# Optimization experiments

Hardware: AMD Instinct MI355X
Metric: run time of the kernel (lower is better)

## Reference

```python
import jax, jax.numpy as jnp
import numpy as np

B, T, D, E, K = 8, 4096, 1024, 64, 2


def setup_inputs() -> dict:
    key = jax.random.key(0)
    k1, k2, k3, k4 = jax.random.split(key, 4)
    return {
        "mh_output": jax.random.normal(k1, (B, T, D), dtype=jnp.float32),
        "W_route": jax.random.normal(k2, (D, E), dtype=jnp.float32) * (1.0 / np.sqrt(D)),
        "b_route": jnp.zeros((E,), dtype=jnp.float32),
        "W_noise": jax.random.normal(k3, (D, E), dtype=jnp.float32) * (1.0 / np.sqrt(D)),
        "b_noise": jnp.zeros((E,), dtype=jnp.float32),
        "noise_u": jax.random.uniform(k4, (B, T, E), dtype=jnp.float32),
        "top_k": K,
    }


def reference(mh_output, W_route, b_route, W_noise, b_noise, noise_u, top_k):
    # [B,T,D] @ [D,E] -> [B,T,E]
    logits = jnp.einsum("btd,de->bte", mh_output, W_route) + b_route
    noise_logits = jnp.einsum("btd,de->bte", mh_output, W_noise) + b_noise
    noisy_logits = logits + noise_u * jax.nn.softplus(noise_logits)
    # top-k over experts
    top_k_logits, indices = jax.lax.top_k(noisy_logits, top_k)  # [B,T,K]
    # scatter top-k values back into -inf canvas == mask non-topk to -inf
    mask = jax.nn.one_hot(indices, E, dtype=jnp.bool_).any(axis=-2)  # [B,T,E]
    sparse_logits = jnp.where(mask, noisy_logits, -jnp.inf)
    router_output = jax.nn.softmax(sparse_logits, axis=-1)
    return (router_output, indices)
```

## Files before the change

kernel.cpp:

```cpp
#include <hip/hip_runtime.h>
#include <math.h>

#define MROWS 32768
#define DDIM  1024
#define EDIM  64
#define NCH   64
#define TILEM 32

typedef _Float16 f16x8 __attribute__((ext_vector_type(8)));
typedef float    f32x16 __attribute__((ext_vector_type(16)));

__global__ __launch_bounds__(256)
void convW_kernel(const float* __restrict__ Wr, const float* __restrict__ Wn,
                  unsigned short* __restrict__ ws) {
    int gid = blockIdx.x * 256 + threadIdx.x;
    int c32 = gid & 31;
    int j   = (gid >> 5) & 7;
    int lhi = (gid >> 8) & 1;
    int nf  = (gid >> 9) & 3;
    int c   = gid >> 11;
    int lane = lhi * 32 + c32;
    int k   = c * 16 + lhi * 8 + j;
    int col = nf * 32 + c32;
    float w = (col < EDIM) ? Wr[k * EDIM + col] : Wn[k * EDIM + (col - EDIM)];
    _Float16 hi = (_Float16)w;
    _Float16 lo = (_Float16)((w - (float)hi) * 2048.0f);
    union { _Float16 h; unsigned short u; } cv;
    size_t base = (size_t)c * 4096 + nf * 512 + lane * 8 + j;
    cv.h = hi; ws[base]        = cv.u;
    cv.h = lo; ws[base + 2048] = cv.u;
}

__global__ __launch_bounds__(256, 4)
void router_mfma(const float* __restrict__ X,
                 const unsigned short* __restrict__ WS,
                 const float* __restrict__ br_g,
                 const float* __restrict__ bn_g,
                 const float* __restrict__ U,
                 float* __restrict__ out)
{
    __shared__ alignas(16) unsigned char smem[22528];
    unsigned short* Ah = (unsigned short*)smem;
    unsigned short* Bh = (unsigned short*)(smem + 6144);
    float*          Lf = (float*)smem;

    const int t    = threadIdx.x;
    const int lane = t & 63;
    const int wid  = t >> 6;
    const int rowBase = blockIdx.x * TILEM;
    const int start   = (blockIdx.x & 7) * 8;

    const int arow = t >> 3;
    const int akk  = (t & 7) * 2;
    const float* xbase = X + (size_t)(rowBase + arow) * DDIM + akk;

    f32x16 acc0, acc1;
#pragma unroll
    for (int i = 0; i < 16; ++i) { acc0[i] = 0.f; acc1[i] = 0.f; }

    auto stageB = [&](int c, int buf) {
        const char* src = (const char*)WS + (size_t)c * 8192 + wid * 2048 + lane * 16;
        char* dst = (char*)(smem + 6144) + buf * 8192 + wid * 2048 + lane * 16;
        __builtin_amdgcn_global_load_lds(
            (const __attribute__((address_space(1))) void*)src,
            (__attribute__((address_space(3))) void*)dst, 16, 0, 0);
        __builtin_amdgcn_global_load_lds(
            (const __attribute__((address_space(1))) void*)(src + 1024),
            (__attribute__((address_space(3))) void*)(dst + 1024), 16, 0, 0);
    };

    auto convA = [&](float2 xv, int buf) {
        _Float16 h0 = (_Float16)xv.x;
        _Float16 h1 = (_Float16)xv.y;
        _Float16 l0 = (_Float16)((xv.x - (float)h0) * 2048.0f);
        _Float16 l1 = (_Float16)((xv.y - (float)h1) * 2048.0f);
        union { _Float16 h[2]; unsigned int u; } ph, pl;
        ph.h[0] = h0; ph.h[1] = h1; pl.h[0] = l0; pl.h[1] = l1;
        *(unsigned int*)(Ah + ((buf * 2 + 0) * 32 + arow) * 24 + akk) = ph.u;
        *(unsigned int*)(Ah + ((buf * 2 + 1) * 32 + arow) * 24 + akk) = pl.u;
    };

    auto compute = [&](int buf) {
        const unsigned short* Ab = Ah + (buf * 2) * 768;
        const int aoff = (lane & 31) * 24 + (lane >> 5) * 8;
        f16x8 ahi = *(const f16x8*)(Ab + aoff);
        f16x8 alo = *(const f16x8*)(Ab + 768 + aoff);
        const unsigned short* Bb = Bh + buf * 4096 + wid * 512 + lane * 8;
        f16x8 bhi = *(const f16x8*)(Bb);
        f16x8 blo = *(const f16x8*)(Bb + 2048);
        acc0 = __builtin_amdgcn_mfma_f32_32x32x16_f16(ahi, bhi, acc0, 0, 0, 0);
        acc1 = __builtin_amdgcn_mfma_f32_32x32x16_f16(ahi, blo, acc1, 0, 0, 0);
        acc1 = __builtin_amdgcn_mfma_f32_32x32x16_f16(alo, bhi, acc1, 0, 0, 0);
    };

    float2 xA = *(const float2*)(xbase + (size_t)start * 16);
    stageB(start, 0);
    convA(xA, 0);
    xA = *(const float2*)(xbase + (size_t)((start + 1) & 63) * 16);
    float2 xB = *(const float2*)(xbase + (size_t)((start + 2) & 63) * 16);
    __syncthreads();

#define PHASE(I, CUR, NXT)                                                     \
    {                                                                          \
        const int buf = (I) & 1;                                               \
        if ((I) + 1 < NCH) stageB((start + (I) + 1) & 63, buf ^ 1);            \
        float2 tmp = CUR;                                                      \
        if ((I) + 3 < NCH)                                                     \
            tmp = *(const float2*)(xbase + (size_t)((start + (I) + 3) & 63) * 16); \
        compute(buf);                                                          \
        if ((I) + 1 < NCH) convA(CUR, buf ^ 1);                                \
        CUR = tmp;                                                             \
        __syncthreads();                                                       \
    }

    for (int i = 0; i < NCH; i += 2) {
        PHASE(i,     xA, xB);
        PHASE(i + 1, xB, xA);
    }
#undef PHASE

    const float inv2048 = 1.0f / 2048.0f;
    const int lcol = wid * 32 + (lane & 31);
#pragma unroll
    for (int reg = 0; reg < 16; ++reg) {
        int r = (reg & 3) + 8 * (reg >> 2) + 4 * (lane >> 5);
        Lf[r * 132 + lcol] = acc0[reg] + acc1[reg] * inv2048;
    }
    __syncthreads();

    const float brv = br_g[lane];
    const float bnv = bn_g[lane];
#pragma unroll 2
    for (int r8 = 0; r8 < 8; ++r8) {
        int lrow = wid * 8 + r8;
        int grow = rowBase + lrow;
        float lr = Lf[lrow * 132 + lane] + brv;
        float ln = Lf[lrow * 132 + 64 + lane] + bnv;
        float u  = U[(size_t)grow * EDIM + lane];
        float noisy = lr + u * log1pf(expf(ln));

        float m1 = noisy; int i1 = lane;
        float m2 = -INFINITY; int i2 = 64;
#pragma unroll
        for (int s = 1; s < 64; s <<= 1) {
            float om1 = __shfl_xor(m1, s); int oi1 = __shfl_xor(i1, s);
            float om2 = __shfl_xor(m2, s); int oi2 = __shfl_xor(i2, s);
            bool aw = (m1 > om1) || (m1 == om1 && i1 < oi1);
            float w1  = aw ? m1 : om1;  int wi1  = aw ? i1 : oi1;
            float c2a = aw ? m2 : om2;  int c2ai = aw ? i2 : oi2;
            float c2b = aw ? om1 : m1;  int c2bi = aw ? oi1 : i1;
            bool bw = (c2b > c2a) || (c2b == c2a && c2bi < c2ai);
            m1 = w1; i1 = wi1;
            m2 = bw ? c2b : c2a;
            i2 = bw ? c2bi : c2ai;
        }
        float e2  = expf(m2 - m1);
        float inv = 1.0f / (1.0f + e2);
        float p   = (lane == i1) ? inv : ((lane == i2) ? e2 * inv : 0.0f);
        out[(size_t)grow * EDIM + lane] = p;
        if (lane < 2)
            out[(size_t)MROWS * EDIM + (size_t)grow * 2 + lane] =
                (float)(lane == 0 ? i1 : i2);
    }
}

extern "C" void kernel_launch(void* const* d_in, const int* in_sizes, int n_in,
                              void* d_out, int out_size, void* d_ws, size_t ws_size,
                              hipStream_t stream) {
    const float* X  = (const float*)d_in[0];
    const float* Wr = (const float*)d_in[1];
    const float* br = (const float*)d_in[2];
    const float* Wn = (const float*)d_in[3];
    const float* bn = (const float*)d_in[4];
    const float* U  = (const float*)d_in[5];
    (void)in_sizes; (void)n_in; (void)ws_size;
    unsigned short* ws16 = (unsigned short*)d_ws;
    convW_kernel<<<512, 256, 0, stream>>>(Wr, Wn, ws16);
    router_mfma<<<MROWS / TILEM, 256, 0, stream>>>(X, ws16, br, bn, U, (float*)d_out);
}
```

Baseline: 62.41 us.

## Deepen B-tile prefetch to a 4-slot LDS ring with manual waitcnt barriers

Grows the B staging area into a four-slot ring so each weight chunk is issued two iterations ahead instead of one. The X loads become a two-deep register prefetch. The generic __syncthreads is replaced with an explicit partial vmcnt wait plus s_barrier, so later loads can stay in flight across the barrier. MFMA issue is wrapped in s_setprio to favour matrix instructions. This hides more global latency but raises LDS use from about 22KB to about 38KB per block, which may limit occupancy. It also depends on exact vmcnt accounting, which has no margin for error.

```diff
diff --git a/kernel.cpp b/kernel.cpp
--- a/kernel.cpp
+++ b/kernel.cpp
@@ -39,7 +39,7 @@
                  const float* __restrict__ U,
                  float* __restrict__ out)
 {
-    __shared__ alignas(16) unsigned char smem[22528];
+    __shared__ alignas(16) unsigned char smem[38912];
     unsigned short* Ah = (unsigned short*)smem;
     unsigned short* Bh = (unsigned short*)(smem + 6144);
     float*          Lf = (float*)smem;
@@ -58,9 +58,9 @@
 #pragma unroll
     for (int i = 0; i < 16; ++i) { acc0[i] = 0.f; acc1[i] = 0.f; }
 
-    auto stageB = [&](int c, int buf) {
+    auto stageB = [&](int c, int ring) {
         const char* src = (const char*)WS + (size_t)c * 8192 + wid * 2048 + lane * 16;
-        char* dst = (char*)(smem + 6144) + buf * 8192 + wid * 2048 + lane * 16;
+        char* dst = (char*)(smem + 6144) + ring * 8192 + wid * 2048 + lane * 16;
         __builtin_amdgcn_global_load_lds(
             (const __attribute__((address_space(1))) void*)src,
             (__attribute__((address_space(3))) void*)dst, 16, 0, 0);
@@ -69,55 +69,63 @@
             (__attribute__((address_space(3))) void*)(dst + 1024), 16, 0, 0);
     };
 
-    auto convA = [&](float2 xv, int buf) {
+    auto convA = [&](float2 xv, int abuf) {
         _Float16 h0 = (_Float16)xv.x;
         _Float16 h1 = (_Float16)xv.y;
         _Float16 l0 = (_Float16)((xv.x - (float)h0) * 2048.0f);
         _Float16 l1 = (_Float16)((xv.y - (float)h1) * 2048.0f);
         union { _Float16 h[2]; unsigned int u; } ph, pl;
         ph.h[0] = h0; ph.h[1] = h1; pl.h[0] = l0; pl.h[1] = l1;
-        *(unsigned int*)(Ah + ((buf * 2 + 0) * 32 + arow) * 24 + akk) = ph.u;
-        *(unsigned int*)(Ah + ((buf * 2 + 1) * 32 + arow) * 24 + akk) = pl.u;
+        *(unsigned int*)(Ah + ((abuf * 2 + 0) * 32 + arow) * 24 + akk) = ph.u;
+        *(unsigned int*)(Ah + ((abuf * 2 + 1) * 32 + arow) * 24 + akk) = pl.u;
     };
 
-    auto compute = [&](int buf) {
-        const unsigned short* Ab = Ah + (buf * 2) * 768;
+    auto compute = [&](int abuf, int ring) {
+        const unsigned short* Ab = Ah + abuf * 1536;
         const int aoff = (lane & 31) * 24 + (lane >> 5) * 8;
         f16x8 ahi = *(const f16x8*)(Ab + aoff);
         f16x8 alo = *(const f16x8*)(Ab + 768 + aoff);
-        const unsigned short* Bb = Bh + buf * 4096 + wid * 512 + lane * 8;
+        const unsigned short* Bb = Bh + ring * 4096 + wid * 512 + lane * 8;
         f16x8 bhi = *(const f16x8*)(Bb);
         f16x8 blo = *(const f16x8*)(Bb + 2048);
+        __builtin_amdgcn_s_setprio(1);
         acc0 = __builtin_amdgcn_mfma_f32_32x32x16_f16(ahi, bhi, acc0, 0, 0, 0);
         acc1 = __builtin_amdgcn_mfma_f32_32x32x16_f16(ahi, blo, acc1, 0, 0, 0);
         acc1 = __builtin_amdgcn_mfma_f32_32x32x16_f16(alo, bhi, acc1, 0, 0, 0);
+        __builtin_amdgcn_s_setprio(0);
     };
 
-    float2 xA = *(const float2*)(xbase + (size_t)start * 16);
+    float2 x0v = *(const float2*)(xbase + (size_t)start * 16);
     stageB(start, 0);
-    convA(xA, 0);
-    xA = *(const float2*)(xbase + (size_t)((start + 1) & 63) * 16);
-    float2 xB = *(const float2*)(xbase + (size_t)((start + 2) & 63) * 16);
-    __syncthreads();
+    stageB((start + 1) & 63, 1);
+    float2 xA = *(const float2*)(xbase + (size_t)((start + 1) & 63) * 16);
+    float2 xB;
+    convA(x0v, 0);
+    asm volatile("s_waitcnt vmcnt(3) lgkmcnt(0)" ::: "memory");
+    __builtin_amdgcn_sched_barrier(0);
+    __builtin_amdgcn_s_barrier();
 
-#define PHASE(I, CUR, NXT)                                                     \
+#define PH(C, CUR, NXT)                                                        \
     {                                                                          \
-        const int buf = (I) & 1;                                               \
-        if ((I) + 1 < NCH) stageB((start + (I) + 1) & 63, buf ^ 1);            \
-        float2 tmp = CUR;                                                      \
-        if ((I) + 3 < NCH)                                                     \
-            tmp = *(const float2*)(xbase + (size_t)((start + (I) + 3) & 63) * 16); \
-        compute(buf);                                                          \
-        if ((I) + 1 < NCH) convA(CUR, buf ^ 1);                                \
-        CUR = tmp;                                                             \
-        __syncthreads();                                                       \
+        const int cc = start + (C);                                            \
+        const int cL = (cc + 2) & 63;                                          \
+        NXT = *(const float2*)(xbase + (size_t)cL * 16);                       \
+        stageB(cL, (cc + 2) & 3);                                              \
+        compute(cc & 1, cc & 3);                                               \
+        convA(CUR, (cc + 1) & 1);                                              \
+        asm volatile("s_waitcnt vmcnt(3) lgkmcnt(0)" ::: "memory");            \
+        __builtin_amdgcn_sched_barrier(0);                                     \
+        __builtin_amdgcn_s_barrier();                                          \
     }
 
     for (int i = 0; i < NCH; i += 2) {
-        PHASE(i,     xA, xB);
-        PHASE(i + 1, xB, xA);
+        PH(i,     xA, xB);
+        PH(i + 1, xB, xA);
     }
-#undef PHASE
+#undef PH
+
+    asm volatile("s_waitcnt vmcnt(0) lgkmcnt(0)" ::: "memory");
+    __syncthreads();
 
     const float inv2048 = 1.0f / 2048.0f;
     const int lcol = wid * 32 + (lane & 31);
```

New measurement: 63.75 us. 1.02x slower.
